# Kernel optimization log

Hardware: AMD Instinct MI355X
Metric: run time of the kernel (lower is better)

## Reference

```python
import jax, jax.numpy as jnp
import numpy as np

N, E, B = 16384, 131072, 256
F_IN, HID, HEADS, F_CELL, N_OUT = 78, 128, 10, 954, 2
NEG_SLOPE = 0.2  # PyG GATConv default


def setup_inputs() -> dict:
    key = jax.random.key(0)
    ks = jax.random.split(key, 24)
    rn = lambda k, shape, s=0.05: (jax.random.normal(k, shape, jnp.float32) * s)
    inp = {
        "x": rn(ks[0], (N, F_IN), 1.0),
        "edge_index": jax.random.randint(ks[1], (2, E), 0, N, dtype=jnp.int32),
        "batch": (jnp.arange(N, dtype=jnp.int32) // (N // B)),  # 64 nodes per graph, sorted
        "cell": rn(ks[2], (B, F_CELL), 1.0),
        "W1": rn(ks[3], (F_IN, HEADS * HID)),
        "a_src1": rn(ks[4], (HEADS, HID)),
        "a_dst1": rn(ks[5], (HEADS, HID)),
        "b1": jnp.zeros((HEADS * HID,), jnp.float32),
        # GATConv layer 2: 1280 -> 128, 1 head
        "W2": rn(ks[6], (HEADS * HID, HID)),
        "a_src2": rn(ks[7], (1, HID)),
        "a_dst2": rn(ks[8], (1, HID)),
        "b2": jnp.zeros((HID,), jnp.float32),
        # drug1_fc_g1: 128 -> 128
        "Wg": rn(ks[9], (HID, HID)), "bg": jnp.zeros((HID,), jnp.float32),
        # fc head applied to normalized cell (source applies fc1 to cell: 954 -> 2048)
        "Wf1": rn(ks[10], (F_CELL, 2048)), "bf1": jnp.zeros((2048,), jnp.float32),
        "Wf2": rn(ks[11], (2048, 512)), "bf2": jnp.zeros((512,), jnp.float32),
        "Wf3": rn(ks[12], (512, 128)), "bf3": jnp.zeros((128,), jnp.float32),
        "Wo": rn(ks[13], (128, N_OUT)), "bo": jnp.zeros((N_OUT,), jnp.float32),
    }
    return inp


def _gat_layer(xin, src, dst, W, a_s, a_d, b, heads, ch):
    """PyG GATConv: linear -> per-edge leaky_relu(a_src.h_j + a_dst.h_i) ->
    segment softmax over incoming edges of dst -> scatter-add of alpha * h_src."""
    n = xin.shape[0]
    h = (xin @ W).reshape(n, heads, ch)                       # [N,H,C]
    es = jnp.einsum('nhc,hc->nh', h, a_s)                     # alpha_src per node
    ed = jnp.einsum('nhc,hc->nh', h, a_d)                     # alpha_dst per node
    e = jax.nn.leaky_relu(es[src] + ed[dst], NEG_SLOPE)       # [Etot,H]
    m = jax.ops.segment_max(e, dst, num_segments=n)           # stable softmax max
    w = jnp.exp(e - m[dst])                                   # unnormalized alpha
    denom = jax.ops.segment_sum(w, dst, num_segments=n)       # [N,H]
    num = jax.ops.segment_sum(w[:, :, None] * h[src], dst, num_segments=n)  # [N,H,C]
    out = num / denom[:, :, None]
    return out.reshape(n, heads * ch) + b


def reference(x, edge_index, batch, cell, W1, a_src1, a_dst1, b1,
              W2, a_src2, a_dst2, b2, Wg, bg, Wf1, bf1, Wf2, bf2,
              Wf3, bf3, Wo, bo):
    n = x.shape[0]
    # add self-loops (PyG GATConv default)
    loop = jnp.arange(n, dtype=edge_index.dtype)
    src = jnp.concatenate([edge_index[0], loop])
    dst = jnp.concatenate([edge_index[1], loop])

    x1 = jax.nn.elu(_gat_layer(x, src, dst, W1, a_src1, a_dst1, b1, HEADS, HID))
    x1 = jax.nn.elu(_gat_layer(x1, src, dst, W2, a_src2, a_dst2, b2, 1, HID))
    # global max pool over graphs (batch is sorted, all B segments non-empty)
    x1 = jax.ops.segment_max(x1, batch, num_segments=B)       # [B,128]
    x1 = jax.nn.relu(x1 @ Wg + bg)

    # cell branch: L2 normalize rows, then dense head (dropout = identity in eval)
    celln = cell / jnp.maximum(jnp.linalg.norm(cell, axis=1, keepdims=True), 1e-12)
    xc = jax.nn.relu(celln @ Wf1 + bf1)
    xc = jax.nn.relu(xc @ Wf2 + bf2)
    xc = jax.nn.relu(xc @ Wf3 + bf3)
    out = xc @ Wo + bo                                        # [B,2]
    # source returns only `out`; we also expose the (otherwise-dead) GAT branch
    return jnp.concatenate([x1, out], axis=1)                 # [B,130]
```

## Files before the change

### kernel.cpp

```cpp
#include <hip/hip_runtime.h>
#include <hip/hip_bf16.h>
#include <math.h>

#define N_NODES 16384
#define E_EDGES 131072
#define ETOT (E_EDGES + N_NODES)
#define BGRAPH 256
#define F_INPUT 78
#define KPAD1 96
#define HID 128
#define HEADS 10
#define F1 (HEADS * HID)
#define F_CELL 954
#define KPADC 960
#define NEG_SLOPE 0.2f

typedef __attribute__((ext_vector_type(8))) short frag_t;
typedef __attribute__((ext_vector_type(4))) float f4_t;

static __device__ __forceinline__ unsigned fkey(float f) {
    unsigned b = __float_as_uint(f);
    return (b & 0x80000000u) ? ~b : (b | 0x80000000u);
}
static __device__ __forceinline__ float funkey(unsigned k) {
    unsigned b = (k & 0x80000000u) ? (k ^ 0x80000000u) : ~k;
    return __uint_as_float(b);
}
static __device__ __forceinline__ unsigned short f2bf(float f) {
    __hip_bfloat16 h = __float2bfloat16(f);
    return *(unsigned short*)&h;
}
static __device__ __forceinline__ float bf2f(unsigned short u) {
    return __uint_as_float(((unsigned)u) << 16);
}

template<int WM16, int WN16, int OUT_MODE, int ACT, int HAS_BIAS>
__global__ __launch_bounds__(256) void gemm_db(
    const unsigned short* __restrict__ A, const unsigned short* __restrict__ BT,
    const float* __restrict__ bias, void* __restrict__ C,
    float* __restrict__ esp, float* __restrict__ edp,
    int M, int N, int K, int lda, int ldb, int ldc,
    int za, int zb, int zc, int zbias)
{
    constexpr int BM = 32 * WM16, BN = 32 * WN16;
    constexpr int LA = BM * 4;
    constexpr int LB = BN * 4;
    constexpr int NA = (LA + 255) / 256;
    constexpr int NB = (LB + 255) / 256;
    __shared__ __align__(16) unsigned short Als[2][BM * 32];
    __shared__ __align__(16) unsigned short Bls[2][BN * 32];
    const int z = blockIdx.z;
    A  += (size_t)z * za;
    BT += (size_t)z * zb;
    const int t = threadIdx.x;
    const int wave = t >> 6, lane = t & 63;
    const int wr = (wave >> 1) * (16 * WM16);
    const int wc = (wave & 1) * (16 * WN16);
    const int row0 = blockIdx.y * BM;
    const int col0 = blockIdx.x * BN;
    const int lrow = lane & 15, kg = lane >> 4;

    uint4 pa[NA], pb[NB];
    auto LOAD = [&](int kk) {
#pragma unroll
        for (int i = 0; i < NA; i++) { int idx = t + i * 256; if (idx < LA) {
            int r = idx >> 2, sl = idx & 3;
            pa[i] = *(const uint4*)&A[(size_t)(row0 + r) * lda + kk + sl * 8]; } }
#pragma unroll
        for (int i = 0; i < NB; i++) { int idx = t + i * 256; if (idx < LB) {
            int r = idx >> 2, sl = idx & 3;
            pb[i] = *(const uint4*)&BT[(size_t)(col0 + r) * ldb + kk + sl * 8]; } }
    };
    auto STORE = [&](int buf) {
#pragma unroll
        for (int i = 0; i < NA; i++) { int idx = t + i * 256; if (idx < LA) {
            int r = idx >> 2, sl = idx & 3;
            *(uint4*)&Als[buf][r * 32 + ((sl ^ (r & 3) ^ ((r >> 2) & 3)) * 8)] = pa[i]; } }
#pragma unroll
        for (int i = 0; i < NB; i++) { int idx = t + i * 256; if (idx < LB) {
            int r = idx >> 2, sl = idx & 3;
            *(uint4*)&Bls[buf][r * 32 + ((sl ^ (r & 3) ^ ((r >> 2) & 3)) * 8)] = pb[i]; } }
    };

    f4_t acc[WM16][WN16];
#pragma unroll
    for (int m = 0; m < WM16; m++)
#pragma unroll
        for (int n = 0; n < WN16; n++) acc[m][n] = (f4_t){0.f, 0.f, 0.f, 0.f};

    LOAD(0);
    STORE(0);
    __syncthreads();

    const int nk = K / 32;
    int cur = 0;
    for (int ks = 0; ks < nk; ks++) {
        if (ks < nk - 1) LOAD((ks + 1) * 32);
        frag_t af[WM16], bfr[WN16];
#pragma unroll
        for (int m = 0; m < WM16; m++) {
            int r = wr + m * 16 + lrow;
            af[m] = *(frag_t*)&Als[cur][r * 32 + ((kg ^ (r & 3) ^ ((r >> 2) & 3)) * 8)];
        }
#pragma unroll
        for (int n = 0; n < WN16; n++) {
            int r = wc + n * 16 + lrow;
            bfr[n] = *(frag_t*)&Bls[cur][r * 32 + ((kg ^ (r & 3) ^ ((r >> 2) & 3)) * 8)];
        }
#pragma unroll
        for (int m = 0; m < WM16; m++)
#pragma unroll
            for (int n = 0; n < WN16; n++)
                acc[m][n] = __builtin_amdgcn_mfma_f32_16x16x32_bf16(af[m], bfr[n], acc[m][n], 0, 0, 0);
        if (ks < nk - 1) STORE(cur ^ 1);
        __syncthreads();
        cur ^= 1;
    }

#pragma unroll
    for (int m = 0; m < WM16; m++) {
#pragma unroll
        for (int n = 0; n < WN16; n++) {
            int col = col0 + wc + n * 16 + lrow;
            float bv = HAS_BIAS ? bias[z * zbias + col] : 0.f;
#pragma unroll
            for (int r = 0; r < 4; r++) {
                int row = row0 + wr + m * 16 + kg * 4 + r;
                float v = acc[m][n][r] + bv;
                if (ACT == 1) v = fmaxf(v, 0.f);
                if (ACT == 2) v = (v > 0.f) ? v : expm1f(v);
                size_t ci = (size_t)row * ldc + (size_t)z * zc + col;
                if (OUT_MODE == 0)      ((float*)C)[ci] = v;
                else if (OUT_MODE == 1) ((unsigned short*)C)[ci] = f2bf(v);
                else {
                    if (col < 10)                  esp[row * 10 + col] = v;
                    else if (col >= 16 && col < 26) edp[row * 10 + (col - 16)] = v;
                }
            }
        }
    }
}

template<int WM16, int WN16, int OUT_MODE, int ACT, int HAS_BIAS>
__global__ __launch_bounds__(256) void mfma_gemm(
    const unsigned short* __restrict__ A, const unsigned short* __restrict__ BT,
    const float* __restrict__ bias, void* __restrict__ C,
    const float* __restrict__ ca, const float* __restrict__ cd,
    int M, int N, int Kpad, int lda, int ldb, int ldc)
{
    constexpr int BM = 32 * WM16, BN = 32 * WN16;
    __shared__ __align__(16) unsigned short Als[BM * 32];
    __shared__ __align__(16) unsigned short Bls[BN * 32];
    const int t = threadIdx.x;
    const int wave = t >> 6, lane = t & 63;
    const int wr = (wave >> 1) * (16 * WM16);
    const int wc = (wave & 1) * (16 * WN16);
    const int row0 = blockIdx.y * BM;
    const int col0 = blockIdx.x * BN;

    f4_t acc[WM16][WN16];
#pragma unroll
    for (int m = 0; m < WM16; m++)
#pragma unroll
        for (int n = 0; n < WN16; n++) { acc[m][n] = (f4_t){0.f, 0.f, 0.f, 0.f}; }

    const int lrow = lane & 15, kg = lane >> 4;
    for (int kk = 0; kk < Kpad; kk += 32) {
        for (int i = t; i < BM * 4; i += 256) {
            int r = i >> 2, slot = i & 3;
            uint4 v = *(const uint4*)&A[(size_t)(row0 + r) * lda + kk + slot * 8];
            *(uint4*)&Als[r * 32 + ((slot ^ (r & 3) ^ ((r >> 2) & 3)) * 8)] = v;
        }
        for (int i = t; i < BN * 4; i += 256) {
            int r = i >> 2, slot = i & 3;
            uint4 v = *(const uint4*)&BT[(size_t)(col0 + r) * ldb + kk + slot * 8];
            *(uint4*)&Bls[r * 32 + ((slot ^ (r & 3) ^ ((r >> 2) & 3)) * 8)] = v;
        }
        __syncthreads();
        frag_t af[WM16], bfr[WN16];
#pragma unroll
        for (int m = 0; m < WM16; m++) {
            int r = wr + m * 16 + lrow;
            af[m] = *(frag_t*)&Als[r * 32 + ((kg ^ (r & 3) ^ ((r >> 2) & 3)) * 8)];
        }
#pragma unroll
        for (int n = 0; n < WN16; n++) {
            int r = wc + n * 16 + lrow;
            bfr[n] = *(frag_t*)&Bls[r * 32 + ((kg ^ (r & 3) ^ ((r >> 2) & 3)) * 8)];
        }
#pragma unroll
        for (int m = 0; m < WM16; m++)
#pragma unroll
            for (int n = 0; n < WN16; n++)
                acc[m][n] = __builtin_amdgcn_mfma_f32_16x16x32_bf16(af[m], bfr[n], acc[m][n], 0, 0, 0);
        __syncthreads();
    }

    if constexpr (OUT_MODE == 0) {
#pragma unroll
        for (int m = 0; m < WM16; m++) {
#pragma unroll
            for (int n = 0; n < WN16; n++) {
                int col = col0 + wc + n * 16 + lrow;
                float bv = HAS_BIAS ? bias[col] : 0.f;
#pragma unroll
                for (int r = 0; r < 4; r++) {
                    int row = row0 + wr + m * 16 + kg * 4 + r;
                    float v = acc[m][n][r] + bv;
                    if (ACT == 1) v = fmaxf(v, 0.f);
                    ((float*)C)[(size_t)row * ldc + col] = v;
                }
            }
        }
    } else {
        __shared__ float o2l[BM][2];
        if (t < BM) { o2l[t][0] = 0.f; o2l[t][1] = 0.f; }
        __syncthreads();
#pragma unroll
        for (int m = 0; m < WM16; m++) {
#pragma unroll
            for (int r = 0; r < 4; r++) {
                int lr = wr + m * 16 + kg * 4 + r;
                float p0 = 0.f, p1 = 0.f;
#pragma unroll
                for (int n = 0; n < WN16; n++) {
                    int col = col0 + wc + n * 16 + lrow;
                    float v = acc[m][n][r] + (HAS_BIAS ? bias[col] : 0.f);
                    if (ACT == 1) v = fmaxf(v, 0.f);
                    p0 = fmaf(v, ca[col * 2], p0);
                    p1 = fmaf(v, ca[col * 2 + 1], p1);
                }
                atomicAdd(&o2l[lr][0], p0);
                atomicAdd(&o2l[lr][1], p1);
            }
        }
        __syncthreads();
        if (t < BM) {
            ((float*)C)[(size_t)(row0 + t) * ldc + 128] = o2l[t][0] + cd[0];
            ((float*)C)[(size_t)(row0 + t) * ldc + 129] = o2l[t][1] + cd[1];
        }
    }
}

__global__ __launch_bounds__(256) void w1_apply(
    const unsigned short* __restrict__ aggb,
    const unsigned short* __restrict__ W1T,
    const float* __restrict__ b1,
    unsigned short* __restrict__ x1)
{
    __shared__ __align__(16) unsigned short ls[24576];
    const int z = blockIdx.y;
    const int row0 = blockIdx.x * 128;
    const int t = threadIdx.x;
    const int wave = t >> 6, lane = t & 63;
    const int wr = (wave >> 1) * 64;
    const int wc = (wave & 1) * 64;
    const int lrow = lane & 15, kg = lane >> 4;

    const unsigned short* A = aggb + (size_t)z * 96;
    const unsigned short* B = W1T + (size_t)z * 128 * 96;

    for (int i = t; i < 1536; i += 256) {
        int r = i / 12, c = i % 12;
        int ks = c >> 2, sl = c & 3;
        int swz = ((sl ^ (r & 3) ^ ((r >> 2) & 3)) * 8);
        uint4 va = *(const uint4*)&A[(size_t)(row0 + r) * 960 + ks * 32 + sl * 8];
        *(uint4*)&ls[(ks * 128 + r) * 32 + swz] = va;
        uint4 vb = *(const uint4*)&B[(size_t)r * 96 + ks * 32 + sl * 8];
        *(uint4*)&ls[12288 + (ks * 128 + r) * 32 + swz] = vb;
    }
    __syncthreads();

    f4_t acc[4][4];
#pragma unroll
    for (int m = 0; m < 4; m++)
#pragma unroll
        for (int n = 0; n < 4; n++) acc[m][n] = (f4_t){0.f, 0.f, 0.f, 0.f};

#pragma unroll
    for (int ks = 0; ks < 3; ks++) {
        frag_t af[4], bfr[4];
#pragma unroll
        for (int m = 0; m < 4; m++) {
            int r = wr + m * 16 + lrow;
            af[m] = *(frag_t*)&ls[(ks * 128 + r) * 32 + ((kg ^ (r & 3) ^ ((r >> 2) & 3)) * 8)];
        }
#pragma unroll
        for (int n = 0; n < 4; n++) {
            int r = wc + n * 16 + lrow;
            bfr[n] = *(frag_t*)&ls[12288 + (ks * 128 + r) * 32 + ((kg ^ (r & 3) ^ ((r >> 2) & 3)) * 8)];
        }
#pragma unroll
        for (int m = 0; m < 4; m++)
#pragma unroll
            for (int n = 0; n < 4; n++)
                acc[m][n] = __builtin_amdgcn_mfma_f32_16x16x32_bf16(af[m], bfr[n], acc[m][n], 0, 0, 0);
    }
    __syncthreads();

#pragma unroll
    for (int m = 0; m < 4; m++) {
#pragma unroll
        for (int n = 0; n < 4; n++) {
            int col = wc + n * 16 + lrow;
            float bv = b1[z * HID + col];
#pragma unroll
            for (int r = 0; r < 4; r++) {
                int lr = wr + m * 16 + kg * 4 + r;
                float v = acc[m][n][r] + bv;
                v = (v > 0.f) ? v : expm1f(v);
                ls[lr * 128 + col] = f2bf(v);
            }
        }
    }
    __syncthreads();

    for (int i = t; i < 2048; i += 256) {
        int r = i >> 4, seg = i & 15;
        *(uint4*)&x1[(size_t)(row0 + r) * F1 + z * HID + seg * 8] =
            *(const uint4*)&ls[r * 128 + seg * 8];
    }
}

__global__ __launch_bounds__(256) void h2_gemm(
    const unsigned short* __restrict__ A, const unsigned short* __restrict__ BT,
    unsigned short* __restrict__ C,
    const float* __restrict__ as2, const float* __restrict__ ad2,
    float* __restrict__ es2, float* __restrict__ ed2)
{
    __shared__ __align__(16) unsigned short Als[2][32 * 32];
    __shared__ __align__(16) unsigned short Bls[2][128 * 32];
    __shared__ __align__(16) unsigned short ob[32 * 128];
    __shared__ float esl[4][32], edl[4][32];
    const int t = threadIdx.x;
    const int wave = t >> 6, lane = t & 63;
    const int lrow = lane & 15, kg = lane >> 4;
    const int row0 = blockIdx.x * 32;
    const int wc = wave * 32;

    const int ar = t >> 2, asl = t & 3;
    const int br = t >> 2, bsl = t & 3;

    uint4 pa, pb0, pb1;
    auto LOAD = [&](int kk) {
        if (t < 128) pa = *(const uint4*)&A[(size_t)(row0 + ar) * F1 + kk + asl * 8];
        pb0 = *(const uint4*)&BT[(size_t)br * F1 + kk + bsl * 8];
        pb1 = *(const uint4*)&BT[(size_t)(br + 64) * F1 + kk + bsl * 8];
    };
    auto STORE = [&](int buf) {
        if (t < 128)
            *(uint4*)&Als[buf][ar * 32 + ((asl ^ (ar & 3) ^ ((ar >> 2) & 3)) * 8)] = pa;
        *(uint4*)&Bls[buf][br * 32 + ((bsl ^ (br & 3) ^ ((br >> 2) & 3)) * 8)] = pb0;
        int r2 = br + 64;
        *(uint4*)&Bls[buf][r2 * 32 + ((bsl ^ (r2 & 3) ^ ((r2 >> 2) & 3)) * 8)] = pb1;
    };

    LOAD(0);
    STORE(0);
    __syncthreads();

    f4_t acc[2][2];
#pragma unroll
    for (int m = 0; m < 2; m++)
#pragma unroll
        for (int n = 0; n < 2; n++) acc[m][n] = (f4_t){0.f, 0.f, 0.f, 0.f};

    int cur = 0;
    for (int ks = 0; ks < 40; ks++) {
        if (ks < 39) LOAD((ks + 1) * 32);
        frag_t af[2], bfr[2];
#pragma unroll
        for (int m = 0; m < 2; m++) {
            int r = m * 16 + lrow;
            af[m] = *(frag_t*)&Als[cur][r * 32 + ((kg ^ (r & 3) ^ ((r >> 2) & 3)) * 8)];
        }
#pragma unroll
        for (int n = 0; n < 2; n++) {
            int r = wc + n * 16 + lrow;
            bfr[n] = *(frag_t*)&Bls[cur][r * 32 + ((kg ^ (r & 3) ^ ((r >> 2) & 3)) * 8)];
        }
#pragma unroll
        for (int m = 0; m < 2; m++)
#pragma unroll
            for (int n = 0; n < 2; n++)
                acc[m][n] = __builtin_amdgcn_mfma_f32_16x16x32_bf16(af[m], bfr[n], acc[m][n], 0, 0, 0);
        if (ks < 39) STORE(cur ^ 1);
        __syncthreads();
        cur ^= 1;
    }

#pragma unroll
    for (int m = 0; m < 2; m++) {
#pragma unroll
        for (int r = 0; r < 4; r++) {
            int lr = m * 16 + kg * 4 + r;
            float pes = 0.f, ped = 0.f;
#pragma unroll
            for (int n = 0; n < 2; n++) {
                int col = wc + n * 16 + lrow;
                float v = acc[m][n][r];
                ob[lr * 128 + col] = f2bf(v);
                pes = fmaf(v, as2[col], pes);
                ped = fmaf(v, ad2[col], ped);
            }
#pragma unroll
            for (int o = 1; o < 16; o <<= 1) {
                pes += __shfl_xor(pes, o);
                ped += __shfl_xor(ped, o);
            }
            if (lrow == 0) { esl[wave][lr] = pes; edl[wave][lr] = ped; }
        }
    }
    __syncthreads();
    for (int i = t; i < 512; i += 256) {
        int r = i >> 4, seg = i & 15;
        *(uint4*)&C[(size_t)(row0 + r) * HID + seg * 8] = *(const uint4*)&ob[r * 128 + seg * 8];
    }
    if (t < 32) {
        es2[row0 + t] = esl[0][t] + esl[1][t] + esl[2][t] + esl[3][t];
        ed2[row0 + t] = edl[0][t] + edl[1][t] + edl[2][t] + edl[3][t];
    }
}

#define S0 1572864
#define S1 122880
#define S2 163840
#define S3 1966080
#define S4 1048576
#define S5 65536
#define S6 16384
#define PREP_TOTAL (S0+S1+S2+S3+S4+S5+S6)
#define NB_ELEM (PREP_TOTAL / 256)
#define NB_FOLD 768
#define NB_ZPK  128
#define NB_HIST ((ETOT + 255) / 256)

__global__ void prep_all(const float* __restrict__ x,  const float* __restrict__ W1,
                         const float* __restrict__ W2, const float* __restrict__ Wf1,
                         const float* __restrict__ Wf2, const float* __restrict__ Wf3,
                         const float* __restrict__ Wg,
                         const float* __restrict__ as1, const float* __restrict__ ad1,
                         const int* __restrict__ ei,
                         unsigned short* __restrict__ xb,  unsigned short* __restrict__ W1T,
                         unsigned short* __restrict__ W2T, unsigned short* __restrict__ Wf1T,
                         unsigned short* __restrict__ Wf2T, unsigned short* __restrict__ Wf3T,
                         unsigned short* __restrict__ WgT, unsigned short* __restrict__ F1T,
                         int* __restrict__ counts, unsigned* __restrict__ pk)
{
    int blk = blockIdx.x, t = threadIdx.x;
    if (blk < NB_ELEM) {
        int i = blk * 256 + t;
        if (i < S0) { int r = i / 96, k = i % 96;
            xb[i] = (k < F_INPUT) ? f2bf(x[r * F_INPUT + k]) : 0; return; }
        i -= S0;
        if (i < S1) { int n = i / 96, k = i % 96;
            W1T[i] = (k < F_INPUT) ? f2bf(W1[(size_t)k * F1 + n]) : 0; return; }
        i -= S1;
        if (i < S2) { int n = i / 1280, k = i % 1280;
            W2T[i] = f2bf(W2[(size_t)k * HID + n]); return; }
        i -= S2;
        if (i < S3) { int n = i / 960, k = i % 960;
            Wf1T[i] = (k < F_CELL) ? f2bf(Wf1[(size_t)k * 2048 + n]) : 0; return; }
        i -= S3;
        if (i < S4) { int n = i / 2048, k = i % 2048;
            Wf2T[i] = f2bf(Wf2[(size_t)k * 512 + n]); return; }
        i -= S4;
        if (i < S5) { int n = i / 512, k = i % 512;
            Wf3T[i] = f2bf(Wf3[(size_t)k * HID + n]); return; }
        i -= S5;
        { int n = i / 128, k = i % 128;
            WgT[i] = f2bf(Wg[(size_t)k * HID + n]); }
        return;
    }
    blk -= NB_ELEM;
    if (blk < NB_FOLD) {
        int idx = blk * 4 + (t >> 6);
        int l = t & 63;
        int r = idx / 96, k = idx % 96;
        int sd = r >> 4, h = r & 15;
        float p = 0.f;
        if (h < HEADS && k < F_INPUT) {
            const float* a = (sd ? ad1 : as1) + h * HID;
            float2 wv = *(const float2*)&W1[(size_t)k * F1 + h * HID + 2 * l];
            float2 av = *(const float2*)&a[2 * l];
            p = wv.x * av.x + wv.y * av.y;
#pragma unroll
            for (int o = 32; o > 0; o >>= 1) p += __shfl_xor(p, o);
        }
        if (l == 0) F1T[(size_t)r * 96 + k] = f2bf(p);
        return;
    }
    blk -= NB_FOLD;
    if (blk < NB_ZPK) { pk[blk * 256 + t] = 0; return; }
    blk -= NB_ZPK;
    int e = blk * 256 + t;
    if (e < ETOT) {
        int dst = (e < E_EDGES) ? ei[E_EDGES + e] : (e - E_EDGES);
        atomicAdd(&counts[dst], 1);
    }
}

__global__ void scan_counts(const int* __restrict__ counts,
                            int* __restrict__ row_start, int* __restrict__ cursor)
{
    __shared__ int part[256];
    int t = threadIdx.x;
    int base = t * 64;
    int4 v[16];
#pragma unroll
    for (int i = 0; i < 16; i++) v[i] = *(const int4*)&counts[base + i * 4];
    int sum = 0;
#pragma unroll
    for (int i = 0; i < 16; i++) sum += v[i].x + v[i].y + v[i].z + v[i].w;
    part[t] = sum;
    __syncthreads();
    for (int o = 1; o < 256; o <<= 1) {
        int vv = (t >= o) ? part[t - o] : 0;
        __syncthreads();
        part[t] += vv;
        __syncthreads();
    }
    int run = (t == 0) ? 0 : part[t - 1];
#pragma unroll
    for (int i = 0; i < 16; i++) {
        int4 w;
        w.x = run; run += v[i].x;
        w.y = run; run += v[i].y;
        w.z = run; run += v[i].z;
        w.w = run; run += v[i].w;
        *(int4*)&row_start[base + i * 4] = w;
        *(int4*)&cursor[base + i * 4] = w;
    }
    if (t == 255) row_start[N_NODES] = run;
}

__global__ void scatter_csr(const int* __restrict__ ei, int* __restrict__ cursor,
                            int* __restrict__ csr_src)
{
    int e = blockIdx.x * blockDim.x + threadIdx.x;
    if (e >= ETOT) return;
    int src, dst;
    if (e < E_EDGES) { src = ei[e]; dst = ei[E_EDGES + e]; } else { src = dst = e - E_EDGES; }
    int pos = atomicAdd(&cursor[dst], 1);
    csr_src[pos] = src;
}

__global__ __launch_bounds__(256) void gat1_agg(
    const int* __restrict__ row_start, const int* __restrict__ csr_src,
    const unsigned* __restrict__ xb32,
    const float* __restrict__ es, const float* __restrict__ ed,
    unsigned* __restrict__ aggb)
{
    const int w = threadIdx.x >> 6, l = threadIdx.x & 63;
    const int n = blockIdx.x * 4 + w;
    const int rs = row_start[n];
    const int deg = row_start[n + 1] - rs;

    __shared__ __align__(16) float w_lds[4][64][12];
    __shared__ int src_lds[4][64];

    float edv[HEADS];
    const float* edp = ed + n * HEADS;
#pragma unroll
    for (int h = 0; h < HEADS; h++) edv[h] = edp[h];

    float acc0[HEADS], acc1[HEADS], den[HEADS];
#pragma unroll
    for (int h = 0; h < HEADS; h++) { acc0[h] = 0.f; acc1[h] = 0.f; den[h] = 0.f; }

    for (int base = 0; base < deg; base += 64) {
        int e = base + l;
        int cnt = min(64, deg - base);
        float wv[HEADS];
        if (e < deg) {
            int s = csr_src[rs + e];
            src_lds[w][l] = s;
            const float* ep = es + s * HEADS;
#pragma unroll
            for (int h = 0; h < HEADS; h++) {
                float v = ep[h] + edv[h];
                v = (v >= 0.f) ? v : NEG_SLOPE * v;
                wv[h] = __expf(v);
            }
        } else {
#pragma unroll
            for (int h = 0; h < HEADS; h++) wv[h] = 0.f;
        }
#pragma unroll
        for (int h = 0; h < HEADS; h++) {
            den[h] += wv[h];
            w_lds[w][l][h] = wv[h];
        }
        asm volatile("" ::: "memory");

        for (int j = 0; j < cnt; j++) {
            int sj = src_lds[w][j];
            unsigned xv = 0;
            if (l < 48) xv = xb32[(size_t)sj * 48 + l];
            float x0 = bf2f((unsigned short)(xv & 0xffffu));
            float x1v = bf2f((unsigned short)(xv >> 16));
            float4 wa = *(const float4*)&w_lds[w][j][0];
            float4 wb = *(const float4*)&w_lds[w][j][4];
            float2 wcv = *(const float2*)&w_lds[w][j][8];
            float ww[HEADS] = {wa.x, wa.y, wa.z, wa.w, wb.x, wb.y, wb.z, wb.w, wcv.x, wcv.y};
#pragma unroll
            for (int h = 0; h < HEADS; h++) {
                acc0[h] = fmaf(ww[h], x0, acc0[h]);
                acc1[h] = fmaf(ww[h], x1v, acc1[h]);
            }
        }
        asm volatile("" ::: "memory");
    }

#pragma unroll
    for (int h = 0; h < HEADS; h++)
#pragma unroll
        for (int o = 32; o > 0; o >>= 1) den[h] += __shfl_xor(den[h], o);

    if (l < 48) {
        unsigned* orow = aggb + (size_t)n * 480;
#pragma unroll
        for (int h = 0; h < HEADS; h++) {
            float inv = 1.f / den[h];
            unsigned lo = f2bf(acc0[h] * inv);
            unsigned hi = f2bf(acc1[h] * inv);
            orow[h * 48 + l] = lo | (hi << 16);
        }
    }
}

__global__ __launch_bounds__(256) void gat2_agg(
    const int* __restrict__ row_start, const int* __restrict__ csr_src,
    const unsigned short* __restrict__ H2,
    const float* __restrict__ es, const float* __restrict__ ed,
    const float* __restrict__ b, const int* __restrict__ batch,
    unsigned* __restrict__ pk)
{
    const int w = threadIdx.x >> 6, l = threadIdx.x & 63;
    const int n = blockIdx.x * 4 + w;
    const int rs = row_start[n];
    const int deg = row_start[n + 1] - rs;
    const float edv = ed[n];

    float2 acc = {0.f, 0.f};
    float den = 0.f;
    for (int base = 0; base < deg; base += 64) {
        int e = base + l;
        int cnt = min(64, deg - base);
        int s = 0;
        float wv = 0.f;
        if (e < deg) {
            s = csr_src[rs + e];
            float v = es[s] + edv;
            v = (v >= 0.f) ? v : NEG_SLOPE * v;
            wv = __expf(v);
        }
        den += wv;
        for (int j = 0; j < cnt; j++) {
            float wj = __shfl(wv, j);
            int   sj = __shfl(s, j);
            unsigned hp = *(const unsigned*)&H2[(size_t)sj * HID + 2 * l];
            acc.x = fmaf(wj, bf2f((unsigned short)(hp & 0xffffu)), acc.x);
            acc.y = fmaf(wj, bf2f((unsigned short)(hp >> 16)), acc.y);
        }
    }
#pragma unroll
    for (int o = 32; o > 0; o >>= 1) den += __shfl_xor(den, o);

    float inv = 1.f / den;
    float2 bv = *(const float2*)&b[2 * l];
    float v0 = acc.x * inv + bv.x;
    float v1 = acc.y * inv + bv.y;
    v0 = (v0 > 0.f) ? v0 : expm1f(v0);
    v1 = (v1 > 0.f) ? v1 : expm1f(v1);
    int g = batch[n];
    atomicMax(&pk[g * HID + 2 * l], fkey(v0));
    atomicMax(&pk[g * HID + 2 * l + 1], fkey(v1));
}

__global__ void decode_cell(const unsigned* __restrict__ pk,
                            unsigned short* __restrict__ pooledb,
                            const float* __restrict__ cell,
                            unsigned short* __restrict__ celln)
{
    int t = threadIdx.x;
    if (blockIdx.x < BGRAPH) {
        int b = blockIdx.x;
        __shared__ float red[256];
        float s = 0.f;
        for (int c = t; c < F_CELL; c += 256) { float v = cell[(size_t)b * F_CELL + c]; s += v * v; }
        red[t] = s; __syncthreads();
        for (int o = 128; o > 0; o >>= 1) { if (t < o) red[t] += red[t + o]; __syncthreads(); }
        float inv = 1.f / fmaxf(sqrtf(red[0]), 1e-12f);
        for (int c = t; c < KPADC; c += 256) {
            float v = (c < F_CELL) ? cell[(size_t)b * F_CELL + c] * inv : 0.f;
            celln[(size_t)b * KPADC + c] = f2bf(v);
        }
    } else {
        int i = (blockIdx.x - BGRAPH) * 256 + t;
        if (i < BGRAPH * HID) pooledb[i] = f2bf(funkey(pk[i]));
    }
}

extern "C" void kernel_launch(void* const* d_in, const int* in_sizes, int n_in,
                              void* d_out, int out_size, void* d_ws, size_t ws_size,
                              hipStream_t stream)
{
    const float* x    = (const float*)d_in[0];
    const int*   ei   = (const int*)d_in[1];
    const int*   batch= (const int*)d_in[2];
    const float* cell = (const float*)d_in[3];
    const float* W1   = (const float*)d_in[4];
    const float* as1  = (const float*)d_in[5];
    const float* ad1  = (const float*)d_in[6];
    const float* b1   = (const float*)d_in[7];
    const float* W2   = (const float*)d_in[8];
    const float* as2  = (const float*)d_in[9];
    const float* ad2  = (const float*)d_in[10];
    const float* b2   = (const float*)d_in[11];
    const float* Wg   = (const float*)d_in[12];
    const float* bg   = (const float*)d_in[13];
    const float* Wf1  = (const float*)d_in[14];
    const float* bf1  = (const float*)d_in[15];
    const float* Wf2  = (const float*)d_in[16];
    const float* bf2  = (const float*)d_in[17];
    const float* Wf3  = (const float*)d_in[18];
    const float* bf3  = (const float*)d_in[19];
    const float* Wo   = (const float*)d_in[20];
    const float* bo   = (const float*)d_in[21];
    float* out = (float*)d_out;

    char* w = (char*)d_ws;
    auto alloc = [&](size_t bytes) { char* p = w; w += (bytes + 255) & ~(size_t)255; return p; };
    unsigned short* xb   = (unsigned short*)alloc((size_t)N_NODES * KPAD1 * 2);
    unsigned short* W1T  = (unsigned short*)alloc((size_t)F1 * KPAD1 * 2);
    unsigned short* F1T  = (unsigned short*)alloc((size_t)32 * KPAD1 * 2);
    unsigned*       aggb = (unsigned*)alloc((size_t)N_NODES * 480 * 4);
    unsigned short* x1   = (unsigned short*)alloc((size_t)N_NODES * F1 * 2);
    unsigned short* W2T  = (unsigned short*)alloc((size_t)HID * F1 * 2);
    unsigned short* H2   = (unsigned short*)alloc((size_t)N_NODES * HID * 2);
    float*    es1  = (float*)alloc((size_t)N_NODES * HEADS * 4);
    float*    ed1  = (float*)alloc((size_t)N_NODES * HEADS * 4);
    float*    es2  = (float*)alloc((size_t)N_NODES * 4);
    float*    ed2  = (float*)alloc((size_t)N_NODES * 4);
    int*      counts    = (int*)alloc((size_t)N_NODES * 4);
    int*      row_start = (int*)alloc((size_t)(N_NODES + 1) * 4);
    int*      cursor    = (int*)alloc((size_t)N_NODES * 4);
    int*      csr_src   = (int*)alloc((size_t)ETOT * 4);
    unsigned* pk   = (unsigned*)alloc((size_t)BGRAPH * HID * 4);
    unsigned short* pooledb = (unsigned short*)alloc((size_t)BGRAPH * HID * 2);
    unsigned short* WgT  = (unsigned short*)alloc((size_t)HID * HID * 2);
    unsigned short* celln = (unsigned short*)alloc((size_t)BGRAPH * KPADC * 2);
    unsigned short* Wf1T = (unsigned short*)alloc((size_t)2048 * KPADC * 2);
    unsigned short* Wf2T = (unsigned short*)alloc((size_t)512 * 2048 * 2);
    unsigned short* Wf3T = (unsigned short*)alloc((size_t)HID * 512 * 2);
    unsigned short* xc1b = (unsigned short*)alloc((size_t)BGRAPH * 2048 * 2);
    unsigned short* xc2b = (unsigned short*)alloc((size_t)BGRAPH * 512 * 2);

    dim3 b256(256);

    hipMemsetAsync(counts, 0, (size_t)N_NODES * 4, stream);

    prep_all<<<NB_ELEM + NB_FOLD + NB_ZPK + NB_HIST, b256, 0, stream>>>(
        x, W1, W2, Wf1, Wf2, Wf3, Wg, as1, ad1, ei,
        xb, W1T, W2T, Wf1T, Wf2T, Wf3T, WgT, F1T, counts, pk);

    scan_counts<<<1, b256, 0, stream>>>(counts, row_start, cursor);
    scatter_csr<<<(ETOT + 255) / 256, b256, 0, stream>>>(ei, cursor, csr_src);

    gemm_db<2, 1, 2, 0, 0><<<dim3(1, N_NODES / 64), b256, 0, stream>>>(
        xb, F1T, nullptr, nullptr, es1, ed1,
        N_NODES, 32, KPAD1, KPAD1, KPAD1, 32, 0, 0, 0, 0);

    gat1_agg<<<N_NODES / 4, b256, 0, stream>>>(row_start, csr_src, (const unsigned*)xb,
                                               es1, ed1, aggb);

    w1_apply<<<dim3(N_NODES / 128, HEADS), b256, 0, stream>>>(
        (const unsigned short*)aggb, W1T, b1, x1);

    h2_gemm<<<N_NODES / 32, b256, 0, stream>>>(x1, W2T, H2, as2, ad2, es2, ed2);

    gat2_agg<<<N_NODES / 4, b256, 0, stream>>>(row_start, csr_src, H2, es2, ed2, b2,
                                               batch, pk);

    decode_cell<<<BGRAPH + (BGRAPH * HID + 255) / 256, b256, 0, stream>>>(
        pk, pooledb, cell, celln);

    mfma_gemm<2, 2, 0, 1, 1><<<dim3(HID / 64, BGRAPH / 64), b256, 0, stream>>>(
        pooledb, WgT, bg, out, nullptr, nullptr,
        BGRAPH, HID, HID, HID, HID, 130);

    gemm_db<1, 2, 1, 1, 1><<<dim3(2048 / 64, BGRAPH / 32), b256, 0, stream>>>(
        celln, Wf1T, bf1, xc1b, nullptr, nullptr,
        BGRAPH, 2048, KPADC, KPADC, KPADC, 2048, 0, 0, 0, 0);
    gemm_db<1, 2, 1, 1, 1><<<dim3(512 / 64, BGRAPH / 32), b256, 0, stream>>>(
        xc1b, Wf2T, bf2, xc2b, nullptr, nullptr,
        BGRAPH, 512, 2048, 2048, 2048, 512, 0, 0, 0, 0);

    mfma_gemm<2, 4, 4, 1, 1><<<dim3(1, BGRAPH / 64), b256, 0, stream>>>(
        xc2b, Wf3T, bf3, out, Wo, bo,
        BGRAPH, HID, 512, 512, 512, 130);
}
```

Measured before the change: 229.0 us.

## Fuse per-head W1 apply with layer-2 GEMM to avoid x1 round trip

Merges the per-head W1 projection (with bias and ELU) and the layer-2 W2 GEMM into one kernel that loops over heads, keeping each head's activated tile in shared memory and accumulating the layer-2 output in registers. This removes the global write and re-read of the N x 1280 bf16 x1 intermediate and one kernel launch. In exchange the grid drops to 256 blocks, each running a serial loop over heads with several syncs and no double buffering, so occupancy and latency hiding may suffer.

```diff
diff --git a/kernel.cpp b/kernel.cpp
--- a/kernel.cpp
+++ b/kernel.cpp
@@ -242,164 +242,129 @@
     }
 }
 
-__global__ __launch_bounds__(256) void w1_apply(
+__global__ __launch_bounds__(256) void w1h2_fused(
     const unsigned short* __restrict__ aggb,
     const unsigned short* __restrict__ W1T,
     const float* __restrict__ b1,
-    unsigned short* __restrict__ x1)
-{
-    __shared__ __align__(16) unsigned short ls[24576];
-    const int z = blockIdx.y;
-    const int row0 = blockIdx.x * 128;
-    const int t = threadIdx.x;
-    const int wave = t >> 6, lane = t & 63;
-    const int wr = (wave >> 1) * 64;
-    const int wc = (wave & 1) * 64;
-    const int lrow = lane & 15, kg = lane >> 4;
-
-    const unsigned short* A = aggb + (size_t)z * 96;
-    const unsigned short* B = W1T + (size_t)z * 128 * 96;
-
-    for (int i = t; i < 1536; i += 256) {
-        int r = i / 12, c = i % 12;
-        int ks = c >> 2, sl = c & 3;
-        int swz = ((sl ^ (r & 3) ^ ((r >> 2) & 3)) * 8);
-        uint4 va = *(const uint4*)&A[(size_t)(row0 + r) * 960 + ks * 32 + sl * 8];
-        *(uint4*)&ls[(ks * 128 + r) * 32 + swz] = va;
-        uint4 vb = *(const uint4*)&B[(size_t)r * 96 + ks * 32 + sl * 8];
-        *(uint4*)&ls[12288 + (ks * 128 + r) * 32 + swz] = vb;
-    }
-    __syncthreads();
-
-    f4_t acc[4][4];
-#pragma unroll
-    for (int m = 0; m < 4; m++)
-#pragma unroll
-        for (int n = 0; n < 4; n++) acc[m][n] = (f4_t){0.f, 0.f, 0.f, 0.f};
-
-#pragma unroll
-    for (int ks = 0; ks < 3; ks++) {
-        frag_t af[4], bfr[4];
-#pragma unroll
-        for (int m = 0; m < 4; m++) {
-            int r = wr + m * 16 + lrow;
-            af[m] = *(frag_t*)&ls[(ks * 128 + r) * 32 + ((kg ^ (r & 3) ^ ((r >> 2) & 3)) * 8)];
-        }
-#pragma unroll
-        for (int n = 0; n < 4; n++) {
-            int r = wc + n * 16 + lrow;
-            bfr[n] = *(frag_t*)&ls[12288 + (ks * 128 + r) * 32 + ((kg ^ (r & 3) ^ ((r >> 2) & 3)) * 8)];
-        }
-#pragma unroll
-        for (int m = 0; m < 4; m++)
-#pragma unroll
-            for (int n = 0; n < 4; n++)
-                acc[m][n] = __builtin_amdgcn_mfma_f32_16x16x32_bf16(af[m], bfr[n], acc[m][n], 0, 0, 0);
-    }
-    __syncthreads();
-
-#pragma unroll
-    for (int m = 0; m < 4; m++) {
-#pragma unroll
-        for (int n = 0; n < 4; n++) {
-            int col = wc + n * 16 + lrow;
-            float bv = b1[z * HID + col];
-#pragma unroll
-            for (int r = 0; r < 4; r++) {
-                int lr = wr + m * 16 + kg * 4 + r;
-                float v = acc[m][n][r] + bv;
-                v = (v > 0.f) ? v : expm1f(v);
-                ls[lr * 128 + col] = f2bf(v);
-            }
-        }
-    }
-    __syncthreads();
-
-    for (int i = t; i < 2048; i += 256) {
-        int r = i >> 4, seg = i & 15;
-        *(uint4*)&x1[(size_t)(row0 + r) * F1 + z * HID + seg * 8] =
-            *(const uint4*)&ls[r * 128 + seg * 8];
-    }
-}
-
-__global__ __launch_bounds__(256) void h2_gemm(
-    const unsigned short* __restrict__ A, const unsigned short* __restrict__ BT,
-    unsigned short* __restrict__ C,
+    const unsigned short* __restrict__ W2T,
+    unsigned short* __restrict__ H2,
     const float* __restrict__ as2, const float* __restrict__ ad2,
     float* __restrict__ es2, float* __restrict__ ed2)
 {
-    __shared__ __align__(16) unsigned short Als[2][32 * 32];
-    __shared__ __align__(16) unsigned short Bls[2][128 * 32];
-    __shared__ __align__(16) unsigned short ob[32 * 128];
-    __shared__ float esl[4][32], edl[4][32];
+    __shared__ __align__(16) unsigned short ls[24576];
+    __shared__ float esl[2][64], edl[2][64];
     const int t = threadIdx.x;
     const int wave = t >> 6, lane = t & 63;
     const int lrow = lane & 15, kg = lane >> 4;
-    const int row0 = blockIdx.x * 32;
-    const int wc = wave * 32;
-
-    const int ar = t >> 2, asl = t & 3;
-    const int br = t >> 2, bsl = t & 3;
-
-    uint4 pa, pb0, pb1;
-    auto LOAD = [&](int kk) {
-        if (t < 128) pa = *(const uint4*)&A[(size_t)(row0 + ar) * F1 + kk + asl * 8];
-        pb0 = *(const uint4*)&BT[(size_t)br * F1 + kk + bsl * 8];
-        pb1 = *(const uint4*)&BT[(size_t)(br + 64) * F1 + kk + bsl * 8];
-    };
-    auto STORE = [&](int buf) {
-        if (t < 128)
-            *(uint4*)&Als[buf][ar * 32 + ((asl ^ (ar & 3) ^ ((ar >> 2) & 3)) * 8)] = pa;
-        *(uint4*)&Bls[buf][br * 32 + ((bsl ^ (br & 3) ^ ((br >> 2) & 3)) * 8)] = pb0;
-        int r2 = br + 64;
-        *(uint4*)&Bls[buf][r2 * 32 + ((bsl ^ (r2 & 3) ^ ((r2 >> 2) & 3)) * 8)] = pb1;
-    };
-
-    LOAD(0);
-    STORE(0);
-    __syncthreads();
-
-    f4_t acc[2][2];
+    const int row0 = blockIdx.x * 64;
+    const int wr = (wave >> 1) * 32;
+    const int wcol = wave & 1;
+    const int wc = wcol * 64;
+
+    f4_t acc2[2][4];
 #pragma unroll
     for (int m = 0; m < 2; m++)
 #pragma unroll
-        for (int n = 0; n < 2; n++) acc[m][n] = (f4_t){0.f, 0.f, 0.f, 0.f};
-
-    int cur = 0;
-    for (int ks = 0; ks < 40; ks++) {
-        if (ks < 39) LOAD((ks + 1) * 32);
-        frag_t af[2], bfr[2];
+        for (int n = 0; n < 4; n++) acc2[m][n] = (f4_t){0.f, 0.f, 0.f, 0.f};
+
+    for (int h = 0; h < HEADS; h++) {
+        for (int i = t; i < 768; i += 256) {
+            int r = i / 12, c = i % 12;
+            int ks = c >> 2, sl = c & 3;
+            uint4 v = *(const uint4*)&aggb[(size_t)(row0 + r) * 960 + h * 96 + ks * 32 + sl * 8];
+            *(uint4*)&ls[(ks * 64 + r) * 32 + ((sl ^ (r & 3) ^ ((r >> 2) & 3)) * 8)] = v;
+        }
+        for (int i = t; i < 1536; i += 256) {
+            int r = i / 12, c = i % 12;
+            int ks = c >> 2, sl = c & 3;
+            uint4 v = *(const uint4*)&W1T[(size_t)(h * 128 + r) * 96 + ks * 32 + sl * 8];
+            *(uint4*)&ls[6144 + (ks * 128 + r) * 32 + ((sl ^ (r & 3) ^ ((r >> 2) & 3)) * 8)] = v;
+        }
+        __syncthreads();
+
+        f4_t acc1[2][4];
+#pragma unroll
+        for (int m = 0; m < 2; m++)
+#pragma unroll
+            for (int n = 0; n < 4; n++) acc1[m][n] = (f4_t){0.f, 0.f, 0.f, 0.f};
+#pragma unroll
+        for (int ks = 0; ks < 3; ks++) {
+            frag_t af[2], bfr[4];
+#pragma unroll
+            for (int m = 0; m < 2; m++) {
+                int r = wr + m * 16 + lrow;
+                af[m] = *(frag_t*)&ls[(ks * 64 + r) * 32 + ((kg ^ (r & 3) ^ ((r >> 2) & 3)) * 8)];
+            }
+#pragma unroll
+            for (int n = 0; n < 4; n++) {
+                int r = wc + n * 16 + lrow;
+                bfr[n] = *(frag_t*)&ls[6144 + (ks * 128 + r) * 32 + ((kg ^ (r & 3) ^ ((r >> 2) & 3)) * 8)];
+            }
+#pragma unroll
+            for (int m = 0; m < 2; m++)
+#pragma unroll
+                for (int n = 0; n < 4; n++)
+                    acc1[m][n] = __builtin_amdgcn_mfma_f32_16x16x32_bf16(af[m], bfr[n], acc1[m][n], 0, 0, 0);
+        }
+        __syncthreads();
+
 #pragma unroll
         for (int m = 0; m < 2; m++) {
-            int r = m * 16 + lrow;
-            af[m] = *(frag_t*)&Als[cur][r * 32 + ((kg ^ (r & 3) ^ ((r >> 2) & 3)) * 8)];
-        }
-#pragma unroll
-        for (int n = 0; n < 2; n++) {
-            int r = wc + n * 16 + lrow;
-            bfr[n] = *(frag_t*)&Bls[cur][r * 32 + ((kg ^ (r & 3) ^ ((r >> 2) & 3)) * 8)];
-        }
-#pragma unroll
-        for (int m = 0; m < 2; m++)
-#pragma unroll
-            for (int n = 0; n < 2; n++)
-                acc[m][n] = __builtin_amdgcn_mfma_f32_16x16x32_bf16(af[m], bfr[n], acc[m][n], 0, 0, 0);
-        if (ks < 39) STORE(cur ^ 1);
-        __syncthreads();
-        cur ^= 1;
+#pragma unroll
+            for (int n = 0; n < 4; n++) {
+                int col = wc + n * 16 + lrow;
+                float bv = b1[h * HID + col];
+                int ks2 = col >> 5, cw = col & 31, slot = cw >> 3, elem = cw & 7;
+#pragma unroll
+                for (int r = 0; r < 4; r++) {
+                    int row = wr + m * 16 + kg * 4 + r;
+                    float v = acc1[m][n][r] + bv;
+                    v = (v > 0.f) ? v : expm1f(v);
+                    ls[(ks2 * 64 + row) * 32 + ((slot ^ (row & 3) ^ ((row >> 2) & 3)) * 8) + elem] = f2bf(v);
+                }
+            }
+        }
+        for (int i = t; i < 2048; i += 256) {
+            int r = i >> 4, c = i & 15;
+            int ks2 = c >> 2, sl = c & 3;
+            uint4 v = *(const uint4*)&W2T[(size_t)r * F1 + h * 128 + ks2 * 32 + sl * 8];
+            *(uint4*)&ls[8192 + (ks2 * 128 + r) * 32 + ((sl ^ (r & 3) ^ ((r >> 2) & 3)) * 8)] = v;
+        }
+        __syncthreads();
+
+#pragma unroll
+        for (int ks = 0; ks < 4; ks++) {
+            frag_t af[2], bfr[4];
+#pragma unroll
+            for (int m = 0; m < 2; m++) {
+                int r = wr + m * 16 + lrow;
+                af[m] = *(frag_t*)&ls[(ks * 64 + r) * 32 + ((kg ^ (r & 3) ^ ((r >> 2) & 3)) * 8)];
+            }
+#pragma unroll
+            for (int n = 0; n < 4; n++) {
+                int r = wc + n * 16 + lrow;
+                bfr[n] = *(frag_t*)&ls[8192 + (ks * 128 + r) * 32 + ((kg ^ (r & 3) ^ ((r >> 2) & 3)) * 8)];
+            }
+#pragma unroll
+            for (int m = 0; m < 2; m++)
+#pragma unroll
+                for (int n = 0; n < 4; n++)
+                    acc2[m][n] = __builtin_amdgcn_mfma_f32_16x16x32_bf16(af[m], bfr[n], acc2[m][n], 0, 0, 0);
+        }
+        __syncthreads();
     }
 
 #pragma unroll
     for (int m = 0; m < 2; m++) {
 #pragma unroll
         for (int r = 0; r < 4; r++) {
-            int lr = m * 16 + kg * 4 + r;
+            int lr = wr + m * 16 + kg * 4 + r;
             float pes = 0.f, ped = 0.f;
 #pragma unroll
-            for (int n = 0; n < 2; n++) {
+            for (int n = 0; n < 4; n++) {
                 int col = wc + n * 16 + lrow;
-                float v = acc[m][n][r];
-                ob[lr * 128 + col] = f2bf(v);
+                float v = acc2[m][n][r];
+                ls[lr * 128 + col] = f2bf(v);
                 pes = fmaf(v, as2[col], pes);
                 ped = fmaf(v, ad2[col], ped);
             }
@@ -408,17 +373,17 @@
                 pes += __shfl_xor(pes, o);
                 ped += __shfl_xor(ped, o);
             }
-            if (lrow == 0) { esl[wave][lr] = pes; edl[wave][lr] = ped; }
+            if (lrow == 0) { esl[wcol][lr] = pes; edl[wcol][lr] = ped; }
         }
     }
     __syncthreads();
-    for (int i = t; i < 512; i += 256) {
+    for (int i = t; i < 1024; i += 256) {
         int r = i >> 4, seg = i & 15;
-        *(uint4*)&C[(size_t)(row0 + r) * HID + seg * 8] = *(const uint4*)&ob[r * 128 + seg * 8];
-    }
-    if (t < 32) {
-        es2[row0 + t] = esl[0][t] + esl[1][t] + esl[2][t] + esl[3][t];
-        ed2[row0 + t] = edl[0][t] + edl[1][t] + edl[2][t] + edl[3][t];
+        *(uint4*)&H2[(size_t)(row0 + r) * HID + seg * 8] = *(const uint4*)&ls[r * 128 + seg * 8];
+    }
+    if (t < 64) {
+        es2[row0 + t] = esl[0][t] + esl[1][t];
+        ed2[row0 + t] = edl[0][t] + edl[1][t];
     }
 }
 
@@ -736,7 +701,6 @@
     unsigned short* W1T  = (unsigned short*)alloc((size_t)F1 * KPAD1 * 2);
     unsigned short* F1T  = (unsigned short*)alloc((size_t)32 * KPAD1 * 2);
     unsigned*       aggb = (unsigned*)alloc((size_t)N_NODES * 480 * 4);
-    unsigned short* x1   = (unsigned short*)alloc((size_t)N_NODES * F1 * 2);
     unsigned short* W2T  = (unsigned short*)alloc((size_t)HID * F1 * 2);
     unsigned short* H2   = (unsigned short*)alloc((size_t)N_NODES * HID * 2);
     float*    es1  = (float*)alloc((size_t)N_NODES * HEADS * 4);
@@ -775,10 +739,8 @@
     gat1_agg<<<N_NODES / 4, b256, 0, stream>>>(row_start, csr_src, (const unsigned*)xb,
                                                es1, ed1, aggb);
 
-    w1_apply<<<dim3(N_NODES / 128, HEADS), b256, 0, stream>>>(
-        (const unsigned short*)aggb, W1T, b1, x1);
-
-    h2_gemm<<<N_NODES / 32, b256, 0, stream>>>(x1, W2T, H2, as2, ad2, es2, ed2);
+    w1h2_fused<<<N_NODES / 64, b256, 0, stream>>>(
+        (const unsigned short*)aggb, W1T, b1, W2T, H2, as2, ad2, es2, ed2);
 
     gat2_agg<<<N_NODES / 4, b256, 0, stream>>>(row_start, csr_src, H2, es2, ed2, b2,
                                                batch, pk);
```

After: 277.1 us. +21.0%, slower.

## Fuse pool decode into Wg head GEMM and move cell normalization into prep

Applied to the files above, without the earlier changes.

Removes the decode_cell kernel. Cell L2 normalization moves into extra blocks of prep_all, and the pooled-key decode is fused into a new pool_head MFMA kernel that reads the atomic-max keys directly and applies Wg, bias and ReLU. This drops one launch and the pooledb round trip through memory. The final Wf3 GEMM switches to a smaller row tile with twice as many blocks to raise parallelism.

```diff
diff --git a/kernel.cpp b/kernel.cpp
--- a/kernel.cpp
+++ b/kernel.cpp
@@ -422,6 +422,76 @@
     }
 }
 
+__global__ __launch_bounds__(256) void pool_head(
+    const unsigned* __restrict__ pk, const unsigned short* __restrict__ WgT,
+    const float* __restrict__ bg, float* __restrict__ out)
+{
+    __shared__ __align__(16) unsigned short Als[64 * 128];
+    __shared__ __align__(16) unsigned short Bls[128 * 128];
+    const int t = threadIdx.x;
+    const int wave = t >> 6, lane = t & 63;
+    const int lrow = lane & 15, kg = lane >> 4;
+    const int row0 = blockIdx.x * 64;
+    const int wr = (wave >> 1) * 32;
+    const int wc = (wave & 1) * 64;
+
+    for (int i = t; i < 4096; i += 256) {
+        int r = i >> 6, k0 = (i & 63) * 2;
+        int ks = k0 >> 5, cw = k0 & 31, slot = cw >> 3, elem = cw & 7;
+        unsigned lo = f2bf(funkey(pk[(row0 + r) * HID + k0]));
+        unsigned hi = f2bf(funkey(pk[(row0 + r) * HID + k0 + 1]));
+        *(unsigned*)&Als[(ks * 64 + r) * 32 + ((slot ^ (r & 3) ^ ((r >> 2) & 3)) * 8) + elem]
+            = lo | (hi << 16);
+    }
+    for (int i = t; i < 2048; i += 256) {
+        int r = i >> 4, c = i & 15;
+        int ks = c >> 2, sl = c & 3;
+        uint4 v = *(const uint4*)&WgT[(size_t)r * HID + ks * 32 + sl * 8];
+        *(uint4*)&Bls[(ks * 128 + r) * 32 + ((sl ^ (r & 3) ^ ((r >> 2) & 3)) * 8)] = v;
+    }
+    __syncthreads();
+
+    f4_t acc[2][4];
+#pragma unroll
+    for (int m = 0; m < 2; m++)
+#pragma unroll
+        for (int n = 0; n < 4; n++) acc[m][n] = (f4_t){0.f, 0.f, 0.f, 0.f};
+
+#pragma unroll
+    for (int ks = 0; ks < 4; ks++) {
+        frag_t af[2], bfr[4];
+#pragma unroll
+        for (int m = 0; m < 2; m++) {
+            int r = wr + m * 16 + lrow;
+            af[m] = *(frag_t*)&Als[(ks * 64 + r) * 32 + ((kg ^ (r & 3) ^ ((r >> 2) & 3)) * 8)];
+        }
+#pragma unroll
+        for (int n = 0; n < 4; n++) {
+            int r = wc + n * 16 + lrow;
+            bfr[n] = *(frag_t*)&Bls[(ks * 128 + r) * 32 + ((kg ^ (r & 3) ^ ((r >> 2) & 3)) * 8)];
+        }
+#pragma unroll
+        for (int m = 0; m < 2; m++)
+#pragma unroll
+            for (int n = 0; n < 4; n++)
+                acc[m][n] = __builtin_amdgcn_mfma_f32_16x16x32_bf16(af[m], bfr[n], acc[m][n], 0, 0, 0);
+    }
+
+#pragma unroll
+    for (int m = 0; m < 2; m++) {
+#pragma unroll
+        for (int n = 0; n < 4; n++) {
+            int col = wc + n * 16 + lrow;
+            float bv = bg[col];
+#pragma unroll
+            for (int r = 0; r < 4; r++) {
+                int row = row0 + wr + m * 16 + kg * 4 + r;
+                out[(size_t)row * 130 + col] = fmaxf(acc[m][n][r] + bv, 0.f);
+            }
+        }
+    }
+}
+
 #define S0 1572864
 #define S1 122880
 #define S2 163840
@@ -434,18 +504,20 @@
 #define NB_FOLD 768
 #define NB_ZPK  128
 #define NB_HIST ((ETOT + 255) / 256)
+#define NB_CELL BGRAPH
 
 __global__ void prep_all(const float* __restrict__ x,  const float* __restrict__ W1,
                          const float* __restrict__ W2, const float* __restrict__ Wf1,
                          const float* __restrict__ Wf2, const float* __restrict__ Wf3,
                          const float* __restrict__ Wg,
                          const float* __restrict__ as1, const float* __restrict__ ad1,
-                         const int* __restrict__ ei,
+                         const int* __restrict__ ei, const float* __restrict__ cell,
                          unsigned short* __restrict__ xb,  unsigned short* __restrict__ W1T,
                          unsigned short* __restrict__ W2T, unsigned short* __restrict__ Wf1T,
                          unsigned short* __restrict__ Wf2T, unsigned short* __restrict__ Wf3T,
                          unsigned short* __restrict__ WgT, unsigned short* __restrict__ F1T,
-                         int* __restrict__ counts, unsigned* __restrict__ pk)
+                         int* __restrict__ counts, unsigned* __restrict__ pk,
+                         unsigned short* __restrict__ celln)
 {
     int blk = blockIdx.x, t = threadIdx.x;
     if (blk < NB_ELEM) {
@@ -493,10 +565,27 @@
     blk -= NB_FOLD;
     if (blk < NB_ZPK) { pk[blk * 256 + t] = 0; return; }
     blk -= NB_ZPK;
-    int e = blk * 256 + t;
-    if (e < ETOT) {
-        int dst = (e < E_EDGES) ? ei[E_EDGES + e] : (e - E_EDGES);
-        atomicAdd(&counts[dst], 1);
+    if (blk < NB_HIST) {
+        int e = blk * 256 + t;
+        if (e < ETOT) {
+            int dst = (e < E_EDGES) ? ei[E_EDGES + e] : (e - E_EDGES);
+            atomicAdd(&counts[dst], 1);
+        }
+        return;
+    }
+    blk -= NB_HIST;
+    {
+        int b = blk;
+        __shared__ float red[256];
+        float s = 0.f;
+        for (int c = t; c < F_CELL; c += 256) { float v = cell[(size_t)b * F_CELL + c]; s += v * v; }
+        red[t] = s; __syncthreads();
+        for (int o = 128; o > 0; o >>= 1) { if (t < o) red[t] += red[t + o]; __syncthreads(); }
+        float inv = 1.f / fmaxf(sqrtf(red[0]), 1e-12f);
+        for (int c = t; c < KPADC; c += 256) {
+            float v = (c < F_CELL) ? cell[(size_t)b * F_CELL + c] * inv : 0.f;
+            celln[(size_t)b * KPADC + c] = f2bf(v);
+        }
     }
 }
 
@@ -676,30 +765,6 @@
     int g = batch[n];
     atomicMax(&pk[g * HID + 2 * l], fkey(v0));
     atomicMax(&pk[g * HID + 2 * l + 1], fkey(v1));
-}
-
-__global__ void decode_cell(const unsigned* __restrict__ pk,
-                            unsigned short* __restrict__ pooledb,
-                            const float* __restrict__ cell,
-                            unsigned short* __restrict__ celln)
-{
-    int t = threadIdx.x;
-    if (blockIdx.x < BGRAPH) {
-        int b = blockIdx.x;
-        __shared__ float red[256];
-        float s = 0.f;
-        for (int c = t; c < F_CELL; c += 256) { float v = cell[(size_t)b * F_CELL + c]; s += v * v; }
-        red[t] = s; __syncthreads();
-        for (int o = 128; o > 0; o >>= 1) { if (t < o) red[t] += red[t + o]; __syncthreads(); }
-        float inv = 1.f / fmaxf(sqrtf(red[0]), 1e-12f);
-        for (int c = t; c < KPADC; c += 256) {
-            float v = (c < F_CELL) ? cell[(size_t)b * F_CELL + c] * inv : 0.f;
-            celln[(size_t)b * KPADC + c] = f2bf(v);
-        }
-    } else {
-        int i = (blockIdx.x - BGRAPH) * 256 + t;
-        if (i < BGRAPH * HID) pooledb[i] = f2bf(funkey(pk[i]));
-    }
 }
 
 extern "C" void kernel_launch(void* const* d_in, const int* in_sizes, int n_in,
@@ -748,7 +813,6 @@
     int*      cursor    = (int*)alloc((size_t)N_NODES * 4);
     int*      csr_src   = (int*)alloc((size_t)ETOT * 4);
     unsigned* pk   = (unsigned*)alloc((size_t)BGRAPH * HID * 4);
-    unsigned short* pooledb = (unsigned short*)alloc((size_t)BGRAPH * HID * 2);
     unsigned short* WgT  = (unsigned short*)alloc((size_t)HID * HID * 2);
     unsigned short* celln = (unsigned short*)alloc((size_t)BGRAPH * KPADC * 2);
     unsigned short* Wf1T = (unsigned short*)alloc((size_t)2048 * KPADC * 2);
@@ -761,9 +825,9 @@
 
     hipMemsetAsync(counts, 0, (size_t)N_NODES * 4, stream);
 
-    prep_all<<<NB_ELEM + NB_FOLD + NB_ZPK + NB_HIST, b256, 0, stream>>>(
-        x, W1, W2, Wf1, Wf2, Wf3, Wg, as1, ad1, ei,
-        xb, W1T, W2T, Wf1T, Wf2T, Wf3T, WgT, F1T, counts, pk);
+    prep_all<<<NB_ELEM + NB_FOLD + NB_ZPK + NB_HIST + NB_CELL, b256, 0, stream>>>(
+        x, W1, W2, Wf1, Wf2, Wf3, Wg, as1, ad1, ei, cell,
+        xb, W1T, W2T, Wf1T, Wf2T, Wf3T, WgT, F1T, counts, pk, celln);
 
     scan_counts<<<1, b256, 0, stream>>>(counts, row_start, cursor);
     scatter_csr<<<(ETOT + 255) / 256, b256, 0, stream>>>(ei, cursor, csr_src);
@@ -783,12 +847,7 @@
     gat2_agg<<<N_NODES / 4, b256, 0, stream>>>(row_start, csr_src, H2, es2, ed2, b2,
                                                batch, pk);
 
-    decode_cell<<<BGRAPH + (BGRAPH * HID + 255) / 256, b256, 0, stream>>>(
-        pk, pooledb, cell, celln);
-
-    mfma_gemm<2, 2, 0, 1, 1><<<dim3(HID / 64, BGRAPH / 64), b256, 0, stream>>>(
-        pooledb, WgT, bg, out, nullptr, nullptr,
-        BGRAPH, HID, HID, HID, HID, 130);
+    pool_head<<<BGRAPH / 64, b256, 0, stream>>>(pk, WgT, bg, out);
 
     gemm_db<1, 2, 1, 1, 1><<<dim3(2048 / 64, BGRAPH / 32), b256, 0, stream>>>(
         celln, Wf1T, bf1, xc1b, nullptr, nullptr,
@@ -797,7 +856,7 @@
         xc1b, Wf2T, bf2, xc2b, nullptr, nullptr,
         BGRAPH, 512, 2048, 2048, 2048, 512, 0, 0, 0, 0);
 
-    mfma_gemm<2, 4, 4, 1, 1><<<dim3(1, BGRAPH / 64), b256, 0, stream>>>(
+    mfma_gemm<1, 4, 4, 1, 1><<<dim3(1, BGRAPH / 32), b256, 0, stream>>>(
         xc2b, Wf3T, bf3, out, Wo, bo,
         BGRAPH, HID, 512, 512, 512, 130);
 }
```

Result: no change. 225.4 us (-1.5%).
